# Kernel tuning notes

Hardware: AMD Instinct MI355X
Metric: run time of the kernel (lower is better)

## Reference

```python
import jax, jax.numpy as jnp
import numpy as np

N_NODES = 50000
N_EDGES = 800000
IN_F, EDGE_F, HID, HEADS, OUT_F = 128, 16, 32, 4, 128
NEG_SLOPE = 0.2


def edge_gat_layer(h, ef, src, dst, W, We, al, ar, ae, b, act):
    """One DGL-style EdgeGATConv layer.
    h: [N, Fin], ef: [E, Fe], W: [Fin, H*D], We: [Fe, H*D],
    al/ar/ae: [H, D], b: [H*D]. Returns [N, H*D].
    """
    N = h.shape[0]
    H, D = al.shape
    feat = (h @ W).reshape(N, H, D)                    # [N,H,D]
    fe = (ef @ We).reshape(-1, H, D)                   # [E,H,D]
    el = jnp.einsum('nhd,hd->nh', feat, al)            # [N,H]
    er = jnp.einsum('nhd,hd->nh', feat, ar)            # [N,H]
    ee = jnp.einsum('ehd,hd->eh', fe, ae)              # [E,H]
    e = jax.nn.leaky_relu(el[src] + er[dst] + ee, NEG_SLOPE)  # [E,H]
    # edge softmax over incoming edges of each dst node
    emax = jax.ops.segment_max(e, dst, num_segments=N)        # [N,H]
    ex = jnp.exp(e - emax[dst])                               # [E,H]
    esum = jax.ops.segment_sum(ex, dst, num_segments=N)       # [N,H]
    a = ex / esum[dst]                                        # [E,H]
    msg = feat[src] * a[:, :, None]                           # [E,H,D]
    rst = jax.ops.segment_sum(msg, dst, num_segments=N)       # [N,H,D]
    rst = rst + b.reshape(1, H, D)
    if act:
        rst = jax.nn.relu(rst)
    return rst.reshape(N, H * D)


def _glorot(k, shape):
    fan = shape[0]
    return jax.random.normal(k, shape, dtype=jnp.float32) / np.sqrt(fan)


def setup_inputs() -> dict:
    key = jax.random.key(0)
    ks = jax.random.split(key, 24)
    inp = {
        'h': jax.random.normal(ks[0], (N_NODES, IN_F), dtype=jnp.float32),
        'edge_feats': jax.random.normal(ks[1], (N_EDGES, EDGE_F), dtype=jnp.float32),
        'src': jax.random.randint(ks[2], (N_EDGES,), 0, N_NODES, dtype=jnp.int32),
        'dst': jax.random.randint(ks[3], (N_EDGES,), 0, N_NODES, dtype=jnp.int32),
    }
    # layer 0: IN_F -> HEADS*HID ; layer 1: HEADS*HID -> HEADS*HID ; layer 2: heads=1, OUT_F
    dims = [(IN_F, HEADS, HID), (HEADS * HID, HEADS, HID), (HEADS * HID, 1, OUT_F)]
    ki = 4
    for i, (fin, H, D) in enumerate(dims):
        inp[f'W{i}'] = _glorot(ks[ki], (fin, H * D)); ki += 1
        inp[f'We{i}'] = _glorot(ks[ki], (EDGE_F, H * D)); ki += 1
        inp[f'al{i}'] = _glorot(ks[ki], (H, D)); ki += 1
        inp[f'ar{i}'] = _glorot(ks[ki], (H, D)); ki += 1
        inp[f'ae{i}'] = _glorot(ks[ki], (H, D)); ki += 1
        inp[f'b{i}'] = jnp.zeros((H * D,), dtype=jnp.float32)
    return inp


def reference(h, edge_feats, src, dst,
              W0, We0, al0, ar0, ae0, b0,
              W1, We1, al1, ar1, ae1, b1,
              W2, We2, al2, ar2, ae2, b2):
    h = edge_gat_layer(h, edge_feats, src, dst, W0, We0, al0, ar0, ae0, b0, True)
    h = edge_gat_layer(h, edge_feats, src, dst, W1, We1, al1, ar1, ae1, b1, True)
    h = edge_gat_layer(h, edge_feats, src, dst, W2, We2, al2, ar2, ae2, b2, False)
    return h
```

## Files before the change

kernel.cpp:

```cpp
#include <hip/hip_runtime.h>
#include <hip/hip_fp16.h>
#include <cstdint>

#define NN 50000
#define NE 800000
static constexpr int HD = 128;
static constexpr int EF_DIM = 16;
static constexpr int SCAN_B = 256;
static constexpr int NPARTS = (NN + SCAN_B - 1) / SCAN_B;

typedef _Float16 f16x4 __attribute__((ext_vector_type(4)));
typedef float f32x4 __attribute__((ext_vector_type(4)));

struct RecP {
    int src;
    int e;
    f16x4 p0;
    f16x4 p1;
    _Float16 p2;
    _Float16 pad;
};
union Rec32 { RecP r; float4 v[2]; };

__global__ __launch_bounds__(256) void k_prep(const float* __restrict__ h,
        const float* __restrict__ We0, const float* __restrict__ ae0,
        const float* __restrict__ We1, const float* __restrict__ ae1,
        const float* __restrict__ We2, const float* __restrict__ ae2,
        const float* __restrict__ W0, const float* __restrict__ W1,
        const float* __restrict__ W2,
        int* __restrict__ deg, float* __restrict__ M,
        _Float16* __restrict__ Wht, _Float16* __restrict__ Xh) {
    const int b = blockIdx.x, t = threadIdx.x;
    if (b < 196) {
        int i = b * 256 + t;
        if (i < NN) deg[i] = 0;
        return;
    }
    if (b < 199) {
        int l = b - 196;
        const float* We = (l == 0) ? We0 : (l == 1) ? We1 : We2;
        const float* ae = (l == 0) ? ae0 : (l == 1) ? ae1 : ae2;
        int H = (l == 2) ? 1 : 4, D = (l == 2) ? 128 : 32;
        if (t < EF_DIM * H) {
            int f = t / H, hh = t % H;
            float s = 0.f;
            for (int d = 0; d < D; d++) s += We[f * HD + hh * D + d] * ae[hh * D + d];
            M[l * 64 + f * H + hh] = s;
        }
        return;
    }
    if (b < 391) {
        int i = (b - 199) * 256 + t;
        int l = i >> 14, rem = i & 16383;
        int n = rem >> 7, k = rem & 127;
        const float* W = (l == 0) ? W0 : (l == 1) ? W1 : W2;
        Wht[(size_t)l * 16384 + n * 128 + k] = (_Float16)W[k * 128 + n];
        return;
    }
    {
        int i = (b - 391) * 256 + t;
        if (i < NN * 32) {
            float4 v = ((const float4*)h)[i];
            f16x4 o = {(_Float16)v.x, (_Float16)v.y, (_Float16)v.z, (_Float16)v.w};
            ((f16x4*)Xh)[i] = o;
        }
    }
}


__global__ void k_hist(const int* __restrict__ dst, int* __restrict__ deg) {
    int e = blockIdx.x * blockDim.x + threadIdx.x;
    if (e < NE) atomicAdd(&deg[dst[e]], 1);
}

__global__ __launch_bounds__(SCAN_B) void k_part(const int* __restrict__ deg,
                                                 int* __restrict__ part) {
    __shared__ int s[SCAN_B];
    int t = threadIdx.x;
    int i = blockIdx.x * SCAN_B + t;
    s[t] = (i < NN) ? deg[i] : 0;
    __syncthreads();
    for (int off = SCAN_B / 2; off > 0; off >>= 1) {
        if (t < off) s[t] += s[t + off];
        __syncthreads();
    }
    if (t == 0) part[blockIdx.x] = s[0];
}

__global__ __launch_bounds__(SCAN_B) void k_scanpart(int* __restrict__ part) {
    __shared__ int s[SCAN_B];
    int t = threadIdx.x;
    int v = (t < NPARTS) ? part[t] : 0;
    s[t] = v;
    __syncthreads();
    for (int off = 1; off < SCAN_B; off <<= 1) {
        int u = (t >= off) ? s[t - off] : 0;
        __syncthreads();
        s[t] += u;
        __syncthreads();
    }
    if (t < NPARTS) part[t] = s[t] - v;
}

__global__ __launch_bounds__(SCAN_B) void k_rowptr(const int* __restrict__ deg,
                                                   const int* __restrict__ part,
                                                   int* __restrict__ row_ptr,
                                                   int* __restrict__ cursor) {
    __shared__ int s[SCAN_B];
    int t = threadIdx.x;
    int i = blockIdx.x * SCAN_B + t;
    int v = (i < NN) ? deg[i] : 0;
    s[t] = v;
    __syncthreads();
    for (int off = 1; off < SCAN_B; off <<= 1) {
        int u = (t >= off) ? s[t - off] : 0;
        __syncthreads();
        s[t] += u;
        __syncthreads();
    }
    int excl = s[t] - v + part[blockIdx.x];
    if (i < NN) { row_ptr[i] = excl; cursor[i] = excl; }
    if (i == NN) row_ptr[NN] = NE;
}

__global__ __launch_bounds__(256) void k_scat64(const int* __restrict__ src,
                                                const int* __restrict__ dst,
                                                const float* __restrict__ EFt,
                                                const float* __restrict__ M,
                                                int* __restrict__ cursor,
                                                float4* __restrict__ rec) {
    __shared__ float sM[192];
    int t = threadIdx.x;
    if (t < 192) sM[t] = M[t];
    __syncthreads();
    int e = blockIdx.x * 256 + t;
    if (e >= NE) return;
    float ef[EF_DIM];
    const float4* efp = (const float4*)(EFt + (size_t)e * EF_DIM);
#pragma unroll
    for (int q = 0; q < 4; q++) {
        float4 v = efp[q];
        ef[4 * q] = v.x; ef[4 * q + 1] = v.y; ef[4 * q + 2] = v.z; ef[4 * q + 3] = v.w;
    }
    float o0[4] = {0.f, 0.f, 0.f, 0.f};
    float o1[4] = {0.f, 0.f, 0.f, 0.f};
    float o2 = 0.f;
#pragma unroll
    for (int f = 0; f < EF_DIM; f++) {
        float v = ef[f];
#pragma unroll
        for (int hh = 0; hh < 4; hh++) {
            o0[hh] += v * sM[f * 4 + hh];
            o1[hh] += v * sM[64 + f * 4 + hh];
        }
        o2 += v * sM[128 + f];
    }
    Rec32 u;
    u.r.src = src[e];
    u.r.e = e;
    u.r.p0 = f16x4{(_Float16)o0[0], (_Float16)o0[1], (_Float16)o0[2], (_Float16)o0[3]};
    u.r.p1 = f16x4{(_Float16)o1[0], (_Float16)o1[1], (_Float16)o1[2], (_Float16)o1[3]};
    u.r.p2 = (_Float16)o2;
    u.r.pad = (_Float16)0.f;
    int d = dst[e];
    int pos = atomicAdd(&cursor[d], 1);
    float4* p = rec + (size_t)pos * 4;
    p[0] = u.v[0];
    p[1] = u.v[1];
    p[2] = make_float4(0.f, 0.f, 0.f, 0.f);
    p[3] = make_float4(0.f, 0.f, 0.f, 0.f);
}

__global__ __launch_bounds__(256) void k_segsort2(const int* __restrict__ row_ptr,
                                                  const float4* __restrict__ rec,
                                                  int* __restrict__ ssrc,
                                                  f16x4* __restrict__ ep0,
                                                  f16x4* __restrict__ ep1,
                                                  _Float16* __restrict__ ep2) {
    __shared__ Rec32 seg[4][128];
    const int wave = threadIdx.x >> 6;
    const int lane = threadIdx.x & 63;
    const int n = blockIdx.x * 4 + wave;
    const int start = row_ptr[n];
    const int len = row_ptr[n + 1] - start;
    const bool small = (len > 0 && len <= 128);
    if (small)
        for (int s = lane; s < len; s += 64) {
            seg[wave][s].v[0] = rec[(size_t)(start + s) * 4];
            seg[wave][s].v[1] = rec[(size_t)(start + s) * 4 + 1];
        }
    __syncthreads();
    if (small) {
        for (int s = lane; s < len; s += 64) {
            RecP me = seg[wave][s].r;
            int rank = 0;
            for (int j = 0; j < len; j++) {
                const RecP& o = seg[wave][j].r;
                rank += (o.src < me.src) || (o.src == me.src && o.e < me.e);
            }
            int w = start + rank;
            ssrc[w] = me.src;
            ep0[w] = me.p0;
            ep1[w] = me.p1;
            ep2[w] = me.p2;
        }
    } else if (len > 128) {
        for (int s = lane; s < len; s += 64) {
            Rec32 u;
            u.v[0] = rec[(size_t)(start + s) * 4];
            u.v[1] = rec[(size_t)(start + s) * 4 + 1];
            int w = start + s;
            ssrc[w] = u.r.src;
            ep0[w] = u.r.p0;
            ep1[w] = u.r.p1;
            ep2[w] = u.r.p2;
        }
    }
}


template <int H>
__global__ __launch_bounds__(256) void k_feat(const _Float16* __restrict__ Xh,
                                              const _Float16* __restrict__ Wht,
                                              const float* __restrict__ al,
                                              const float* __restrict__ ar,
                                              _Float16* __restrict__ Fh,
                                              float* __restrict__ el,
                                              float* __restrict__ er) {
    const int t = threadIdx.x;
    const int lane = t & 63;
    const int wv = t >> 6;
    const int l15 = lane & 15;
    const int kg = lane >> 4;
    const int nbase = blockIdx.x * 64;
    const int arow = nbase + wv * 16 + l15;
    const int rclamp = (arow < NN) ? arow : NN - 1;
    const int ksub = kg * 4;
    f16x4 a[8];
#pragma unroll
    for (int kb = 0; kb < 8; kb++)
        a[kb] = *(const f16x4*)(Xh + (size_t)rclamp * 128 + kb * 16 + ksub);

    const int r0 = nbase + wv * 16 + kg * 4;
    float slp[4][H], srp[4][H];
#pragma unroll
    for (int r = 0; r < 4; r++)
#pragma unroll
        for (int hh = 0; hh < H; hh++) { slp[r][hh] = 0.f; srp[r][hh] = 0.f; }

#pragma unroll
    for (int nt = 0; nt < 8; nt++) {
        f32x4 acc = {0.f, 0.f, 0.f, 0.f};
        const int nc = nt * 16 + l15;
        const _Float16* wp = Wht + (size_t)nc * 128;
#pragma unroll
        for (int kb = 0; kb < 8; kb++) {
            f16x4 bf = *(const f16x4*)(wp + kb * 16 + ksub);
            acc = __builtin_amdgcn_mfma_f32_16x16x16f16(a[kb], bf, acc, 0, 0, 0);
        }
        const float alv = al[nc], arv = ar[nc];
        constexpr int HSEL = 0;
        const int hsel = (H == 4) ? (nt >> 1) : HSEL;
#pragma unroll
        for (int r = 0; r < 4; r++) {
            int ro = r0 + r;
            if (ro < NN) Fh[(size_t)ro * 128 + nc] = (_Float16)acc[r];
            slp[r][hsel] += acc[r] * alv;
            srp[r][hsel] += acc[r] * arv;
        }
    }

#pragma unroll
    for (int m = 1; m < 16; m <<= 1)
#pragma unroll
        for (int r = 0; r < 4; r++)
#pragma unroll
            for (int hh = 0; hh < H; hh++) {
                slp[r][hh] += __shfl_xor(slp[r][hh], m);
                srp[r][hh] += __shfl_xor(srp[r][hh], m);
            }

    if (H == 4) {
        int r = l15 >> 2, hh2 = l15 & 3;
        float sv = 0.f, ev = 0.f;
#pragma unroll
        for (int rr = 0; rr < 4; rr++)
#pragma unroll
            for (int hc = 0; hc < H; hc++)
                if (rr == r && hc == hh2) { sv = slp[rr][hc]; ev = srp[rr][hc]; }
        int ro = r0 + r;
        if (ro < NN) { el[ro * 4 + hh2] = sv; er[ro * 4 + hh2] = ev; }
    } else {
        if (l15 < 4) {
            float sv = 0.f, ev = 0.f;
#pragma unroll
            for (int rr = 0; rr < 4; rr++)
                if (rr == l15) { sv = slp[rr][0]; ev = srp[rr][0]; }
            int ro = r0 + l15;
            if (ro < NN) { el[ro] = sv; er[ro] = ev; }
        }
    }
}

template <int H, int D, int OUT16>
__global__ __launch_bounds__(256) void k_node(const int* __restrict__ row_ptr,
                                              const int* __restrict__ ssrc,
                                              const _Float16* __restrict__ ep,
                                              const float* __restrict__ el,
                                              const float* __restrict__ er,
                                              const __half2* __restrict__ Fh,
                                              const float* __restrict__ bias,
                                              float* __restrict__ Rf,
                                              _Float16* __restrict__ Rh,
                                              int act) {
    __shared__ float wlds[4][256];
    const int wave = threadIdx.x >> 6;
    const int lane = threadIdx.x & 63;
    const int n = blockIdx.x * 4 + wave;
    const int start = row_ptr[n];
    const int end = row_ptr[n + 1];
    const int len = end - start;
    const int slots = len * H;
    const int c = 2 * lane;
    const int hcol = c / D;
    float2 b2 = make_float2(bias[c], bias[c + 1]);
    float2 a = make_float2(0.f, 0.f);

    if (len > 0) {
        constexpr int hsh = (H == 4) ? 2 : 0;
        const int hh = lane & (H - 1);
        const float er_j = er[n * H + hh];
        const _Float16* epb = ep + (size_t)start * H;
        float pmax = -3.0e38f, psum = 0.f;

        if (slots <= 256) {
            float* wp = wlds[wave];
            for (int jj = lane; jj < slots; jj += 64) {
                int i = start + (jj >> hsh);
                float x = el[ssrc[i] * H + hh] + er_j + (float)epb[jj];
                x = (x > 0.f) ? x : 0.2f * x;
                wp[jj] = x;
                pmax = fmaxf(pmax, x);
            }
            for (int m = H; m < 64; m <<= 1) pmax = fmaxf(pmax, __shfl_xor(pmax, m));
            for (int jj = lane; jj < slots; jj += 64) {
                float ex = __expf(wp[jj] - pmax);
                wp[jj] = ex;
                psum += ex;
            }
            for (int m = H; m < 64; m <<= 1) psum += __shfl_xor(psum, m);
            const float inv = 1.f / __shfl(psum, hcol);
#pragma unroll 4
            for (int i = start; i < end; i++) {
                float w = wp[(i - start) * H + hcol];
                float2 f2 = __half22float2(Fh[(size_t)ssrc[i] * 64 + lane]);
                a.x += f2.x * w;
                a.y += f2.y * w;
            }
            a.x *= inv;
            a.y *= inv;
        } else {
            for (int jj = lane; jj < slots; jj += 64) {
                int i = start + (jj >> hsh);
                float x = el[ssrc[i] * H + hh] + er_j + (float)epb[jj];
                x = (x > 0.f) ? x : 0.2f * x;
                pmax = fmaxf(pmax, x);
            }
            for (int m = H; m < 64; m <<= 1) pmax = fmaxf(pmax, __shfl_xor(pmax, m));
            for (int jj = lane; jj < slots; jj += 64) {
                int i = start + (jj >> hsh);
                float x = el[ssrc[i] * H + hh] + er_j + (float)epb[jj];
                x = (x > 0.f) ? x : 0.2f * x;
                psum += __expf(x - pmax);
            }
            for (int m = H; m < 64; m <<= 1) psum += __shfl_xor(psum, m);
            const float inv = 1.f / __shfl(psum, hcol);
            const float pm_c = __shfl(pmax, hcol);
            const float er_c = er[n * H + hcol];
            for (int i = start; i < end; i++) {
                int sn = ssrc[i];
                float x = el[sn * H + hcol] + er_c + (float)epb[(i - start) * H + hcol];
                x = (x > 0.f) ? x : 0.2f * x;
                float w = __expf(x - pm_c);
                float2 f2 = __half22float2(Fh[(size_t)sn * 64 + lane]);
                a.x += f2.x * w;
                a.y += f2.y * w;
            }
            a.x *= inv;
            a.y *= inv;
        }
    }

    float2 v = make_float2(a.x + b2.x, a.y + b2.y);
    if (act) { v.x = fmaxf(v.x, 0.f); v.y = fmaxf(v.y, 0.f); }
    if (OUT16)
        ((__half2*)Rh)[(size_t)n * 64 + lane] = __floats2half2_rn(v.x, v.y);
    else
        ((float2*)Rf)[(size_t)n * 64 + lane] = v;
}


extern "C" void kernel_launch(void* const* d_in, const int* in_sizes, int n_in,
                              void* d_out, int out_size, void* d_ws, size_t ws_size,
                              hipStream_t stream) {
    const float* h   = (const float*)d_in[0];
    const float* eft = (const float*)d_in[1];
    const int* src   = (const int*)d_in[2];
    const int* dst   = (const int*)d_in[3];
    auto P = [&](int i) { return (const float*)d_in[i]; };

    float* ws = (float*)d_ws;
    float4* rec    = (float4*)ws;
    _Float16* Fh   = (_Float16*)ws;
    float* el      = ws + 3200000;
    float* er      = ws + 3400000;
    _Float16* Xh   = (_Float16*)(ws + 12800000);
    _Float16* Wht  = (_Float16*)(ws + 16000000);
    _Float16* ep0s = Wht + 3 * 16384;
    _Float16* ep1s = ep0s + (size_t)NE * 4;
    _Float16* ep2s = ep1s + (size_t)NE * 4;
    int* ssrc      = (int*)(ep2s + NE);
    float* M       = (float*)(ssrc + NE);
    int* row_ptr   = (int*)(M + 192);
    int* cursor    = row_ptr + (NN + 1);
    int* deg       = cursor + NN;
    int* part      = deg + NN;
    float* out     = (float*)d_out;

    hipLaunchKernelGGL(k_prep, dim3(391 + (NN * 32 + 255) / 256), dim3(256), 0, stream,
                       h, P(5), P(8), P(11), P(14), P(17), P(20),
                       P(4), P(10), P(16), deg, M, Wht, Xh);
    hipLaunchKernelGGL(k_hist, dim3((NE + 255) / 256), dim3(256), 0, stream, dst, deg);
    hipLaunchKernelGGL(k_part, dim3(NPARTS), dim3(SCAN_B), 0, stream, deg, part);
    hipLaunchKernelGGL(k_scanpart, dim3(1), dim3(SCAN_B), 0, stream, part);
    hipLaunchKernelGGL(k_rowptr, dim3(NPARTS), dim3(SCAN_B), 0, stream,
                       deg, part, row_ptr, cursor);
    hipLaunchKernelGGL(k_scat64, dim3((NE + 255) / 256), dim3(256), 0, stream,
                       src, dst, eft, M, cursor, rec);
    hipLaunchKernelGGL(k_segsort2, dim3(NN / 4), dim3(256), 0, stream,
                       row_ptr, rec, ssrc, (f16x4*)ep0s, (f16x4*)ep1s, ep2s);

    const int FG = (NN + 63) / 64;
    hipLaunchKernelGGL((k_feat<4>), dim3(FG), dim3(256), 0, stream,
                       Xh, Wht, P(6), P(7), Fh, el, er);
    hipLaunchKernelGGL((k_node<4, 32, 1>), dim3(NN / 4), dim3(256), 0, stream,
                       row_ptr, ssrc, ep0s, el, er, (const __half2*)Fh, P(9),
                       nullptr, Xh, 1);
    hipLaunchKernelGGL((k_feat<4>), dim3(FG), dim3(256), 0, stream,
                       Xh, Wht + 16384, P(12), P(13), Fh, el, er);
    hipLaunchKernelGGL((k_node<4, 32, 1>), dim3(NN / 4), dim3(256), 0, stream,
                       row_ptr, ssrc, ep1s, el, er, (const __half2*)Fh, P(15),
                       nullptr, Xh, 1);
    hipLaunchKernelGGL((k_feat<1>), dim3(FG), dim3(256), 0, stream,
                       Xh, Wht + 32768, P(18), P(19), Fh, el, er);
    hipLaunchKernelGGL((k_node<1, 128, 0>), dim3(NN / 4), dim3(256), 0, stream,
                       row_ptr, ssrc, ep2s, el, er, (const __half2*)Fh, P(21),
                       out, nullptr, 0);
}
```

Measured before the change: 391.2 us.

## Process two edges per wave in node aggregation and compact edge records

The node aggregation kernel now splits each wave into two halves that handle alternating edges, each lane gathering four fp16 features (8 bytes) instead of two. The halves are combined with a cross-half shuffle before bias and activation, and normalization moves into the final epilogue. Separately, the scattered edge records shrink from 64 to 32 bytes by dropping the zero padding, which halves scatter write and segsort read traffic, and workspace offsets are compacted. The cost is an extra reduction step and masked work on odd-length tails.

```diff
diff --git a/kernel.cpp b/kernel.cpp
--- a/kernel.cpp
+++ b/kernel.cpp
@@ -164,11 +164,8 @@
     u.r.pad = (_Float16)0.f;
     int d = dst[e];
     int pos = atomicAdd(&cursor[d], 1);
-    float4* p = rec + (size_t)pos * 4;
-    p[0] = u.v[0];
-    p[1] = u.v[1];
-    p[2] = make_float4(0.f, 0.f, 0.f, 0.f);
-    p[3] = make_float4(0.f, 0.f, 0.f, 0.f);
+    rec[(size_t)pos * 2] = u.v[0];
+    rec[(size_t)pos * 2 + 1] = u.v[1];
 }
 
 __global__ __launch_bounds__(256) void k_segsort2(const int* __restrict__ row_ptr,
@@ -186,8 +183,8 @@
     const bool small = (len > 0 && len <= 128);
     if (small)
         for (int s = lane; s < len; s += 64) {
-            seg[wave][s].v[0] = rec[(size_t)(start + s) * 4];
-            seg[wave][s].v[1] = rec[(size_t)(start + s) * 4 + 1];
+            seg[wave][s].v[0] = rec[(size_t)(start + s) * 2];
+            seg[wave][s].v[1] = rec[(size_t)(start + s) * 2 + 1];
         }
     __syncthreads();
     if (small) {
@@ -207,8 +204,8 @@
     } else if (len > 128) {
         for (int s = lane; s < len; s += 64) {
             Rec32 u;
-            u.v[0] = rec[(size_t)(start + s) * 4];
-            u.v[1] = rec[(size_t)(start + s) * 4 + 1];
+            u.v[0] = rec[(size_t)(start + s) * 2];
+            u.v[1] = rec[(size_t)(start + s) * 2 + 1];
             int w = start + s;
             ssrc[w] = u.r.src;
             ep0[w] = u.r.p0;
@@ -308,7 +305,7 @@
                                               const _Float16* __restrict__ ep,
                                               const float* __restrict__ el,
                                               const float* __restrict__ er,
-                                              const __half2* __restrict__ Fh,
+                                              const _Float16* __restrict__ Fh,
                                               const float* __restrict__ bias,
                                               float* __restrict__ Rf,
                                               _Float16* __restrict__ Rh,
@@ -321,10 +318,10 @@
     const int end = row_ptr[n + 1];
     const int len = end - start;
     const int slots = len * H;
-    const int c = 2 * lane;
-    const int hcol = c / D;
-    float2 b2 = make_float2(bias[c], bias[c + 1]);
-    float2 a = make_float2(0.f, 0.f);
+    const int q = lane & 31;
+    const int hq = (H == 4) ? (q >> 3) : 0;
+    float acc4[4] = {0.f, 0.f, 0.f, 0.f};
+    float inv = 0.f;
 
     if (len > 0) {
         constexpr int hsh = (H == 4) ? 2 : 0;
@@ -349,16 +346,22 @@
                 psum += ex;
             }
             for (int m = H; m < 64; m <<= 1) psum += __shfl_xor(psum, m);
-            const float inv = 1.f / __shfl(psum, hcol);
+            inv = 1.f / __shfl(psum, hq);
+
 #pragma unroll 4
-            for (int i = start; i < end; i++) {
-                float w = wp[(i - start) * H + hcol];
-                float2 f2 = __half22float2(Fh[(size_t)ssrc[i] * 64 + lane]);
-                a.x += f2.x * w;
-                a.y += f2.y * w;
-            }
-            a.x *= inv;
-            a.y *= inv;
+            for (int i = start; i < end; i += 2) {
+                int idx = i + (lane >> 5);
+                bool valid = idx < end;
+                int ii = valid ? idx : end - 1;
+                int sn = ssrc[ii];
+                float w = valid ? wp[(ii - start) * H + hq] : 0.f;
+                float2 fv = ((const float2*)Fh)[(size_t)sn * 32 + q];
+                const __half2* hp = (const __half2*)&fv;
+                float2 lo = __half22float2(hp[0]);
+                float2 hi = __half22float2(hp[1]);
+                acc4[0] += lo.x * w; acc4[1] += lo.y * w;
+                acc4[2] += hi.x * w; acc4[3] += hi.y * w;
+            }
         } else {
             for (int jj = lane; jj < slots; jj += 64) {
                 int i = start + (jj >> hsh);
@@ -374,29 +377,49 @@
                 psum += __expf(x - pmax);
             }
             for (int m = H; m < 64; m <<= 1) psum += __shfl_xor(psum, m);
-            const float inv = 1.f / __shfl(psum, hcol);
-            const float pm_c = __shfl(pmax, hcol);
-            const float er_c = er[n * H + hcol];
-            for (int i = start; i < end; i++) {
-                int sn = ssrc[i];
-                float x = el[sn * H + hcol] + er_c + (float)epb[(i - start) * H + hcol];
+            inv = 1.f / __shfl(psum, hq);
+            const float pm_q = __shfl(pmax, hq);
+            const float er_q = er[n * H + hq];
+            for (int i = start; i < end; i += 2) {
+                int idx = i + (lane >> 5);
+                bool valid = idx < end;
+                int ii = valid ? idx : end - 1;
+                int sn = ssrc[ii];
+                float x = el[sn * H + hq] + er_q + (float)epb[(ii - start) * H + hq];
                 x = (x > 0.f) ? x : 0.2f * x;
-                float w = __expf(x - pm_c);
-                float2 f2 = __half22float2(Fh[(size_t)sn * 64 + lane]);
-                a.x += f2.x * w;
-                a.y += f2.y * w;
-            }
-            a.x *= inv;
-            a.y *= inv;
-        }
-    }
-
-    float2 v = make_float2(a.x + b2.x, a.y + b2.y);
-    if (act) { v.x = fmaxf(v.x, 0.f); v.y = fmaxf(v.y, 0.f); }
-    if (OUT16)
-        ((__half2*)Rh)[(size_t)n * 64 + lane] = __floats2half2_rn(v.x, v.y);
-    else
-        ((float2*)Rf)[(size_t)n * 64 + lane] = v;
+                float w = valid ? __expf(x - pm_q) : 0.f;
+                float2 fv = ((const float2*)Fh)[(size_t)sn * 32 + q];
+                const __half2* hp = (const __half2*)&fv;
+                float2 lo = __half22float2(hp[0]);
+                float2 hi = __half22float2(hp[1]);
+                acc4[0] += lo.x * w; acc4[1] += lo.y * w;
+                acc4[2] += hi.x * w; acc4[3] += hi.y * w;
+            }
+        }
+#pragma unroll
+        for (int j = 0; j < 4; j++) acc4[j] += __shfl_xor(acc4[j], 32);
+    }
+
+    if (lane < 32) {
+        float4 bv = ((const float4*)bias)[q];
+        float v0 = acc4[0] * inv + bv.x;
+        float v1 = acc4[1] * inv + bv.y;
+        float v2 = acc4[2] * inv + bv.z;
+        float v3 = acc4[3] * inv + bv.w;
+        if (len == 0) { v0 = bv.x; v1 = bv.y; v2 = bv.z; v3 = bv.w; }
+        if (act) {
+            v0 = fmaxf(v0, 0.f); v1 = fmaxf(v1, 0.f);
+            v2 = fmaxf(v2, 0.f); v3 = fmaxf(v3, 0.f);
+        }
+        if (OUT16) {
+            float2 st;
+            ((__half2*)&st)[0] = __floats2half2_rn(v0, v1);
+            ((__half2*)&st)[1] = __floats2half2_rn(v2, v3);
+            ((float2*)Rh)[(size_t)n * 32 + q] = st;
+        } else {
+            ((float4*)Rf)[(size_t)n * 32 + q] = make_float4(v0, v1, v2, v3);
+        }
+    }
 }
 
 
@@ -414,8 +437,8 @@
     _Float16* Fh   = (_Float16*)ws;
     float* el      = ws + 3200000;
     float* er      = ws + 3400000;
-    _Float16* Xh   = (_Float16*)(ws + 12800000);
-    _Float16* Wht  = (_Float16*)(ws + 16000000);
+    _Float16* Xh   = (_Float16*)(ws + 6400000);
+    _Float16* Wht  = (_Float16*)(ws + 9600000);
     _Float16* ep0s = Wht + 3 * 16384;
     _Float16* ep1s = ep0s + (size_t)NE * 4;
     _Float16* ep2s = ep1s + (size_t)NE * 4;
@@ -444,16 +467,16 @@
     hipLaunchKernelGGL((k_feat<4>), dim3(FG), dim3(256), 0, stream,
                        Xh, Wht, P(6), P(7), Fh, el, er);
     hipLaunchKernelGGL((k_node<4, 32, 1>), dim3(NN / 4), dim3(256), 0, stream,
-                       row_ptr, ssrc, ep0s, el, er, (const __half2*)Fh, P(9),
+                       row_ptr, ssrc, ep0s, el, er, Fh, P(9),
                        nullptr, Xh, 1);
     hipLaunchKernelGGL((k_feat<4>), dim3(FG), dim3(256), 0, stream,
                        Xh, Wht + 16384, P(12), P(13), Fh, el, er);
     hipLaunchKernelGGL((k_node<4, 32, 1>), dim3(NN / 4), dim3(256), 0, stream,
-                       row_ptr, ssrc, ep1s, el, er, (const __half2*)Fh, P(15),
+                       row_ptr, ssrc, ep1s, el, er, Fh, P(15),
                        nullptr, Xh, 1);
     hipLaunchKernelGGL((k_feat<1>), dim3(FG), dim3(256), 0, stream,
                        Xh, Wht + 32768, P(18), P(19), Fh, el, er);
     hipLaunchKernelGGL((k_node<1, 128, 0>), dim3(NN / 4), dim3(256), 0, stream,
-                       row_ptr, ssrc, ep2s, el, er, (const __half2*)Fh, P(21),
+                       row_ptr, ssrc, ep2s, el, er, Fh, P(21),
                        out, nullptr, 0);
 }
```

Result: slower. 406.3 us (+3.9%).
